# Kernel optimization log

Hardware: AMD Instinct MI355X
Metric: run time of the kernel (lower is better)

The kernel has to match this reference:

```python
import jax, jax.numpy as jnp
import numpy as np
import math

H = 16        # num query heads
KV = 4        # num key/value heads
HD = 128      # head_dim
THETA = 10000.0

def _rope(x, cos, sin):
    # x: [B, h, S, HD]; cos/sin: [1, 1, S, HD//2]
    xr, xi = x[..., :HD // 2], x[..., HD // 2:]
    return jnp.concatenate([xr * cos - xi * sin, xr * sin + xi * cos], axis=-1)

def setup_inputs() -> dict:
    key = jax.random.key(0)
    ks = jax.random.split(key, 5)
    B, S, D = 1, 4096, 2048
    s = 1.0 / math.sqrt(D)
    return {
        "hidden_states": jax.random.normal(ks[0], (B, S, D), jnp.float32),
        "Wq": jax.random.normal(ks[1], (D, H * HD), jnp.float32) * s,
        "Wk": jax.random.normal(ks[2], (D, KV * HD), jnp.float32) * s,
        "Wv": jax.random.normal(ks[3], (D, KV * HD), jnp.float32) * s,
        "Wo": jax.random.normal(ks[4], (H * HD, D), jnp.float32) * s,
    }

def reference(hidden_states, Wq, Wk, Wv, Wo):
    B, S, D = hidden_states.shape
    # projections -> [B, h, S, HD]
    q = (hidden_states @ Wq).reshape(B, S, H, HD).transpose(0, 2, 1, 3)
    k = (hidden_states @ Wk).reshape(B, S, KV, HD).transpose(0, 2, 1, 3)
    v = (hidden_states @ Wv).reshape(B, S, KV, HD).transpose(0, 2, 1, 3)
    # rotary embedding (half-split layout, matching the torch module)
    inv_freq = 1.0 / (THETA ** (jnp.arange(0, HD, 2, dtype=jnp.float32) / HD))
    freqs = jnp.arange(S, dtype=jnp.float32)[:, None] * inv_freq[None, :]  # [S, HD//2]
    cos = jnp.cos(freqs)[None, None]
    sin = jnp.sin(freqs)[None, None]
    q = _rope(q, cos, sin)
    k = _rope(k, cos, sin)
    # GQA: repeat KV heads to match query heads
    rep = H // KV
    k = jnp.repeat(k, rep, axis=1)
    v = jnp.repeat(v, rep, axis=1)
    # non-causal scaled dot-product attention (world_size==1 path)
    scores = jnp.einsum('bhqd,bhkd->bhqk', q, k) / math.sqrt(HD)
    w = jax.nn.softmax(scores, axis=-1)
    o = jnp.einsum('bhqk,bhkd->bhqd', w, v)
    o = o.transpose(0, 2, 1, 3).reshape(B, S, H * HD)
    return o @ Wo
```

## Files before the change

kernel.cpp:

```cpp
#include <hip/hip_runtime.h>
#include <math.h>

#define S_LEN 4096
#define D_MODEL 2048
#define N_HEADS 16
#define N_KV 4
#define HEAD_DIM 128
#define KV_D 512
#define QKV_N 3072
#define SM_SHIFT 18.0f

typedef short bf16x8 __attribute__((ext_vector_type(8)));
typedef float f32x4 __attribute__((ext_vector_type(4)));

#if __has_builtin(__builtin_amdgcn_exp2f)
#define EXP2(x) __builtin_amdgcn_exp2f(x)
#else
#define EXP2(x) exp2f(x)
#endif

static __device__ __forceinline__ unsigned short f2b(float f) {
  unsigned int u = __float_as_uint(f);
  unsigned int r = (u + 0x7FFFu + ((u >> 16) & 1u)) >> 16;
  return (unsigned short)r;
}
static __device__ __forceinline__ float b2f(unsigned short h) {
  return __uint_as_float(((unsigned int)h) << 16);
}
static __device__ __forceinline__ unsigned int cvt_pk_bf16(float a, float b) {
  unsigned int r;
  asm("v_cvt_pk_bf16_f32 %0, %1, %2" : "=v"(r) : "v"(a), "v"(b));
  return r;
}

static __device__ __forceinline__ void gload_lds16(const unsigned short* g,
                                                   unsigned short* l) {
  __builtin_amdgcn_global_load_lds(
      (const __attribute__((address_space(1))) void*)g,
      (__attribute__((address_space(3))) void*)l, 16, 0, 0);
}

__global__ __launch_bounds__(256) void prep_kernel(
    const float* __restrict__ X, const float* __restrict__ Wq,
    const float* __restrict__ Wk, const float* __restrict__ Wv,
    const float* __restrict__ Wo, unsigned short* __restrict__ Xb,
    unsigned short* __restrict__ Wqkv, unsigned short* __restrict__ WoT) {
  __shared__ float tile[32][33];
  const int b = blockIdx.x, t = threadIdx.x;
  if (b < 4096) {
    int i = b * 2048 + t * 8;
    float4 a = *(const float4*)(X + i);
    float4 v = *(const float4*)(X + i + 4);
    unsigned short tmp[8] = {f2b(a.x), f2b(a.y), f2b(a.z), f2b(a.w),
                             f2b(v.x), f2b(v.y), f2b(v.z), f2b(v.w)};
    *(uint4*)&Xb[i] = *(uint4*)tmp;
    return;
  }
  int id = b - 4096;
  const float* src;
  unsigned short* dst;
  int N, tc, rowOff;
  if (id < 4096) { src = Wq; dst = Wqkv; N = 2048; tc = 64; rowOff = 0; }
  else if (id < 5120) { id -= 4096; src = Wk; dst = Wqkv; N = 512; tc = 16; rowOff = 2048; }
  else if (id < 6144) { id -= 5120; src = Wv; dst = Wqkv; N = 512; tc = 16; rowOff = 2560; }
  else { id -= 6144; src = Wo; dst = WoT; N = 2048; tc = 64; rowOff = 0; }
  const int c0 = (id % tc) * 32, r0 = (id / tc) * 32;
  const int col = t & 31, rb = t >> 5;
#pragma unroll
  for (int i = 0; i < 4; i++)
    tile[rb + i * 8][col] = src[(size_t)(r0 + rb + i * 8) * N + c0 + col];
  __syncthreads();
#pragma unroll
  for (int i = 0; i < 4; i++)
    dst[(size_t)(rowOff + c0 + rb + i * 8) * 2048 + r0 + col] =
        f2b(tile[col][rb + i * 8]);
}

__global__ __launch_bounds__(256) void bgemm_kernel(
    const unsigned short* __restrict__ A, const unsigned short* __restrict__ Bt,
    void* __restrict__ C, int M, int N, int K, int bf16_out) {
  __shared__ unsigned short As[128 * 32];
  __shared__ unsigned short Bs[128 * 32];

  const int t = threadIdx.x;
  const int w = t >> 6, l = t & 63;
  const int quad = l >> 4, lx = l & 15;
  const int row0 = blockIdx.y * 128, col0 = blockIdx.x * 128;
  const int wr = (w >> 1) * 64, wc = (w & 1) * 64;

  f32x4 acc[4][4];
#pragma unroll
  for (int mt = 0; mt < 4; mt++)
#pragma unroll
    for (int nt = 0; nt < 4; nt++) acc[mt][nt] = (f32x4){0.f, 0.f, 0.f, 0.f};

  for (int kt = 0; kt < K; kt += 32) {
    __syncthreads();
#pragma unroll
    for (int j = 0; j < 2; j++) {
      int ch = w * 128 + j * 64 + l;
      int r = ch >> 2, kc = (ch & 3) * 8;
      gload_lds16(A + (size_t)(row0 + r) * K + kt + kc, &As[ch * 8]);
      gload_lds16(Bt + (size_t)(col0 + r) * K + kt + kc, &Bs[ch * 8]);
    }
    __syncthreads();

    bf16x8 af[4], bfr[4];
#pragma unroll
    for (int mt = 0; mt < 4; mt++)
      af[mt] = *(const bf16x8*)&As[(wr + mt * 16 + lx) * 32 + quad * 8];
#pragma unroll
    for (int nt = 0; nt < 4; nt++)
      bfr[nt] = *(const bf16x8*)&Bs[(wc + nt * 16 + lx) * 32 + quad * 8];
#pragma unroll
    for (int mt = 0; mt < 4; mt++)
#pragma unroll
      for (int nt = 0; nt < 4; nt++)
        acc[mt][nt] = __builtin_amdgcn_mfma_f32_16x16x32_bf16(af[mt], bfr[nt],
                                                              acc[mt][nt], 0, 0, 0);
  }

  if (bf16_out) {
    unsigned short* Cp = (unsigned short*)C;
#pragma unroll
    for (int mt = 0; mt < 4; mt++)
#pragma unroll
      for (int nt = 0; nt < 4; nt++)
#pragma unroll
        for (int r = 0; r < 4; r++) {
          int row = row0 + wr + mt * 16 + quad * 4 + r;
          int col = col0 + wc + nt * 16 + lx;
          Cp[(size_t)row * N + col] = f2b(acc[mt][nt][r]);
        }
  } else {
    float* Cp = (float*)C;
#pragma unroll
    for (int mt = 0; mt < 4; mt++)
#pragma unroll
      for (int nt = 0; nt < 4; nt++)
#pragma unroll
        for (int r = 0; r < 4; r++) {
          int row = row0 + wr + mt * 16 + quad * 4 + r;
          int col = col0 + wc + nt * 16 + lx;
          Cp[(size_t)row * N + col] = acc[mt][nt][r];
        }
  }
}

__global__ __launch_bounds__(256) void rope_kernel(unsigned short* __restrict__ QKV) {
  int id = blockIdx.x * 256 + threadIdx.x;
  int d = id & 63;
  int rem = id >> 6;
  int head = rem % 20;
  int s = rem / 20;
  unsigned short* p;
  float scale;
  if (head < N_HEADS) {
    p = QKV + (size_t)s * QKV_N + head * HEAD_DIM;
    scale = 0.12753139187f;
  } else {
    p = QKV + (size_t)s * QKV_N + 2048 + (head - N_HEADS) * HEAD_DIM;
    scale = 1.0f;
  }
  float inv = exp2f(-(float)d * (13.287712379549449f / 64.0f));
  float ang = (float)s * inv;
  float sn, c;
  sincosf(ang, &sn, &c);
  float xr = b2f(p[d]), xi = b2f(p[d + 64]);
  p[d] = f2b((xr * c - xi * sn) * scale);
  p[d + 64] = f2b((xr * sn + xi * c) * scale);
}

__global__ __launch_bounds__(256) void vtrans_kernel(
    const unsigned short* __restrict__ Vb, unsigned short* __restrict__ Vt) {
  __shared__ unsigned short tile[32][33];
  const int t = threadIdx.x;
  const int c0 = blockIdx.x * 32;
  const int s0 = blockIdx.y * 32;
  const int col = t & 31, rbase = t >> 5;
#pragma unroll
  for (int i = 0; i < 4; i++) {
    int row = rbase + i * 8;
    tile[row][col] = Vb[(size_t)(s0 + row) * QKV_N + c0 + col];
  }
  __syncthreads();
#pragma unroll
  for (int i = 0; i < 4; i++) {
    int row = rbase + i * 8;
    Vt[(size_t)(c0 + row) * S_LEN + s0 + col] = tile[col][row];
  }
}

__global__ __launch_bounds__(256, 2) void attn_kernel(
    const unsigned short* __restrict__ Qb, const unsigned short* __restrict__ Kb,
    const unsigned short* __restrict__ Vt, unsigned short* __restrict__ Ob) {
  __shared__ unsigned short Ks[2][64 * 128];
  __shared__ unsigned short Vs[2][128 * 64];
  __shared__ unsigned short Pt[4][32 * 64];

  const int t = threadIdx.x;
  const int wave = t >> 6;
  const int lane = t & 63;
  const int quad = lane >> 4;
  const int lx = lane & 15;
  const int lx7 = lx & 7;
  const int qt = blockIdx.x;
  const int h = blockIdx.y;
  const int kvh = h >> 2;

  const unsigned short* Kg = Kb + kvh * HEAD_DIM;
  const unsigned short* Vg = Vt + (size_t)(kvh * HEAD_DIM) * S_LEN;

  const unsigned short* Qg =
      Qb + (size_t)(qt * 128 + wave * 32) * QKV_N + h * HEAD_DIM;
  bf16x8 qf[2][4];
#pragma unroll
  for (int qs = 0; qs < 2; qs++)
#pragma unroll
    for (int ks = 0; ks < 4; ks++)
      qf[qs][ks] = *(const bf16x8*)(Qg + (size_t)(qs * 16 + lx) * QKV_N +
                                    (quad << 3) + (ks << 5));

  f32x4 oacc[2][8];
#pragma unroll
  for (int qs = 0; qs < 2; qs++)
#pragma unroll
    for (int dt = 0; dt < 8; dt++) oacc[qs][dt] = (f32x4){0.f, 0.f, 0.f, 0.f};
  float l_st[2] = {0.f, 0.f};

  const unsigned short* kgp[4];
  const unsigned short* vgp[4];
#pragma unroll
  for (int j = 0; j < 4; j++) {
    int ch = (j * 4 + wave) * 64 + lane;
    int r = ch >> 4, c = ch & 15;
    kgp[j] = Kg + (size_t)r * QKV_N + ((c ^ (r & 7)) << 3);
    int d = ch >> 3, c2 = ch & 7;
    vgp[j] = Vg + (size_t)d * S_LEN + ((c2 ^ (d & 7)) << 3);
  }

  auto stage = [&](int kt, int b) {
#pragma unroll
    for (int j = 0; j < 4; j++) {
      int ch = (j * 4 + wave) * 64 + lane;
      gload_lds16(kgp[j] + (size_t)kt * (64 * QKV_N), &Ks[b][ch * 8]);
    }
#pragma unroll
    for (int j = 0; j < 4; j++) {
      int ch = (j * 4 + wave) * 64 + lane;
      gload_lds16(vgp[j] + kt * 64, &Vs[b][ch * 8]);
    }
  };

  stage(0, 0);

  for (int kt = 0; kt < S_LEN / 64; kt++) {
    __syncthreads();
    if (kt + 1 < S_LEN / 64) stage(kt + 1, (kt + 1) & 1);
    const unsigned short* KsC = Ks[kt & 1];
    const unsigned short* VsC = Vs[kt & 1];

#pragma unroll
    for (int ksub = 0; ksub < 4; ksub++) {
      bf16x8 kf[4];
#pragma unroll
      for (int ks = 0; ks < 4; ks++)
        kf[ks] = *(const bf16x8*)&KsC[(ksub * 16 + lx) * 128 +
                                      (((ks * 4 + quad) ^ lx7) << 3)];
#pragma unroll
      for (int qs = 0; qs < 2; qs++) {
        f32x4 a = (f32x4){-SM_SHIFT, -SM_SHIFT, -SM_SHIFT, -SM_SHIFT};
        __builtin_amdgcn_s_setprio(1);
#pragma unroll
        for (int ks = 0; ks < 4; ks++)
          a = __builtin_amdgcn_mfma_f32_16x16x32_bf16(kf[ks], qf[qs][ks], a, 0, 0, 0);
        __builtin_amdgcn_s_setprio(0);
        float p0 = EXP2(a[0]);
        float p1 = EXP2(a[1]);
        float p2 = EXP2(a[2]);
        float p3 = EXP2(a[3]);
        l_st[qs] += (p0 + p1) + (p2 + p3);
        *(uint2*)&Pt[wave][(qs * 16 + lx) * 64 +
                           (((2 * ksub + (quad >> 1)) ^ lx7) << 3) +
                           ((quad & 1) << 2)] =
            make_uint2(cvt_pk_bf16(p0, p1), cvt_pk_bf16(p2, p3));
      }
    }

#pragma unroll
    for (int st = 0; st < 2; st++) {
      const int pc = ((st * 4 + quad) ^ lx7) << 3;
      bf16x8 pb0 = *(const bf16x8*)&Pt[wave][lx * 64 + pc];
      bf16x8 pb1 = *(const bf16x8*)&Pt[wave][(16 + lx) * 64 + pc];
      __builtin_amdgcn_s_setprio(1);
#pragma unroll
      for (int dt = 0; dt < 8; dt++) {
        bf16x8 vf = *(const bf16x8*)&VsC[(dt * 16 + lx) * 64 + pc];
        oacc[0][dt] = __builtin_amdgcn_mfma_f32_16x16x32_bf16(vf, pb0, oacc[0][dt], 0, 0, 0);
        oacc[1][dt] = __builtin_amdgcn_mfma_f32_16x16x32_bf16(vf, pb1, oacc[1][dt], 0, 0, 0);
      }
      __builtin_amdgcn_s_setprio(0);
    }
  }

#pragma unroll
  for (int qs = 0; qs < 2; qs++) {
    float l = l_st[qs];
    l += __shfl_xor(l, 16);
    l += __shfl_xor(l, 32);
    float linv = 1.0f / l;
    unsigned short* ob = Ob +
        (size_t)(qt * 128 + wave * 32 + qs * 16 + lx) * D_MODEL + h * HEAD_DIM +
        quad * 4;
#pragma unroll
    for (int dt = 0; dt < 8; dt++) {
      *(uint2*)&ob[dt * 16] = make_uint2(
          cvt_pk_bf16(oacc[qs][dt][0] * linv, oacc[qs][dt][1] * linv),
          cvt_pk_bf16(oacc[qs][dt][2] * linv, oacc[qs][dt][3] * linv));
    }
  }
}

extern "C" void kernel_launch(void* const* d_in, const int* in_sizes, int n_in,
                              void* d_out, int out_size, void* d_ws,
                              size_t ws_size, hipStream_t stream) {
  const float* X = (const float*)d_in[0];
  const float* Wq = (const float*)d_in[1];
  const float* Wk = (const float*)d_in[2];
  const float* Wv = (const float*)d_in[3];
  const float* Wo = (const float*)d_in[4];
  float* out = (float*)d_out;

  const size_t MB = 1048576;
  char* ws = (char*)d_ws;
  unsigned short* Xb    = (unsigned short*)ws;
  unsigned short* WqkvT = (unsigned short*)(ws + 16 * MB);
  unsigned short* WoT   = (unsigned short*)(ws + 28 * MB);
  unsigned short* QKV   = (unsigned short*)(ws + 36 * MB);
  unsigned short* Vtr   = (unsigned short*)(ws + 60 * MB);
  unsigned short* Ob    = (unsigned short*)(ws + 64 * MB);

  dim3 blk(256);
  prep_kernel<<<14336, blk, 0, stream>>>(X, Wq, Wk, Wv, Wo, Xb, WqkvT, WoT);
  bgemm_kernel<<<dim3(QKV_N / 128, S_LEN / 128), blk, 0, stream>>>(
      Xb, WqkvT, QKV, S_LEN, QKV_N, D_MODEL, 1);
  rope_kernel<<<(S_LEN * 20 * 64) / 256, blk, 0, stream>>>(QKV);
  vtrans_kernel<<<dim3(KV_D / 32, S_LEN / 32), blk, 0, stream>>>(QKV + 2560, Vtr);
  attn_kernel<<<dim3(S_LEN / 128, N_HEADS), blk, 0, stream>>>(
      QKV, QKV + 2048, Vtr, Ob);
  bgemm_kernel<<<dim3(D_MODEL / 128, S_LEN / 128), blk, 0, stream>>>(
      Ob, WoT, out, S_LEN, D_MODEL, D_MODEL, 0);
}
```

Measured before the change: 405.0 us.

## Split K/V waits in attention loop, fuse rope and V transpose, use hw bf16 convert

The attention main loop replaces __syncthreads with explicit vmcnt waits and raw barriers. Only the K half of the prefetched tile is waited on before QK^T, and V is waited on later, before the PV stage, so the V load overlaps the score computation. The rope and V-transpose kernels are merged into one launch, and the software float-to-bf16 rounding is replaced by the v_cvt_pk_bf16 instruction. The manual vmcnt counts depend on exact load ordering, so any compiler reordering or extra memory ops could break correctness.

Result: no change. 401.0 us (-1.0%).

```diff
diff --git a/kernel.cpp b/kernel.cpp
--- a/kernel.cpp
+++ b/kernel.cpp
@@ -19,11 +19,9 @@
 #define EXP2(x) exp2f(x)
 #endif
 
-static __device__ __forceinline__ unsigned short f2b(float f) {
-  unsigned int u = __float_as_uint(f);
-  unsigned int r = (u + 0x7FFFu + ((u >> 16) & 1u)) >> 16;
-  return (unsigned short)r;
-}
+#define SBAR() asm volatile("s_barrier" ::: "memory")
+#define VMCNT(n) asm volatile("s_waitcnt vmcnt(" #n ")" ::: "memory")
+
 static __device__ __forceinline__ float b2f(unsigned short h) {
   return __uint_as_float(((unsigned int)h) << 16);
 }
@@ -31,6 +29,9 @@
   unsigned int r;
   asm("v_cvt_pk_bf16_f32 %0, %1, %2" : "=v"(r) : "v"(a), "v"(b));
   return r;
+}
+static __device__ __forceinline__ unsigned short f2b(float f) {
+  return (unsigned short)cvt_pk_bf16(f, f);
 }
 
 static __device__ __forceinline__ void gload_lds16(const unsigned short* g,
@@ -51,8 +52,8 @@
     int i = b * 2048 + t * 8;
     float4 a = *(const float4*)(X + i);
     float4 v = *(const float4*)(X + i + 4);
-    unsigned short tmp[8] = {f2b(a.x), f2b(a.y), f2b(a.z), f2b(a.w),
-                             f2b(v.x), f2b(v.y), f2b(v.z), f2b(v.w)};
+    unsigned int tmp[4] = {cvt_pk_bf16(a.x, a.y), cvt_pk_bf16(a.z, a.w),
+                           cvt_pk_bf16(v.x, v.y), cvt_pk_bf16(v.z, v.w)};
     *(uint4*)&Xb[i] = *(uint4*)tmp;
     return;
   }
@@ -147,36 +148,38 @@
   }
 }
 
-__global__ __launch_bounds__(256) void rope_kernel(unsigned short* __restrict__ QKV) {
-  int id = blockIdx.x * 256 + threadIdx.x;
-  int d = id & 63;
-  int rem = id >> 6;
-  int head = rem % 20;
-  int s = rem / 20;
-  unsigned short* p;
-  float scale;
-  if (head < N_HEADS) {
-    p = QKV + (size_t)s * QKV_N + head * HEAD_DIM;
-    scale = 0.12753139187f;
-  } else {
-    p = QKV + (size_t)s * QKV_N + 2048 + (head - N_HEADS) * HEAD_DIM;
-    scale = 1.0f;
-  }
-  float inv = exp2f(-(float)d * (13.287712379549449f / 64.0f));
-  float ang = (float)s * inv;
-  float sn, c;
-  sincosf(ang, &sn, &c);
-  float xr = b2f(p[d]), xi = b2f(p[d + 64]);
-  p[d] = f2b((xr * c - xi * sn) * scale);
-  p[d + 64] = f2b((xr * sn + xi * c) * scale);
-}
-
-__global__ __launch_bounds__(256) void vtrans_kernel(
-    const unsigned short* __restrict__ Vb, unsigned short* __restrict__ Vt) {
+__global__ __launch_bounds__(256) void ropev_kernel(
+    unsigned short* __restrict__ QKV, unsigned short* __restrict__ Vt) {
+  const int t = threadIdx.x;
+  if (blockIdx.x < 20480) {
+    int id = blockIdx.x * 256 + t;
+    int d = id & 63;
+    int rem = id >> 6;
+    int head = rem % 20;
+    int s = rem / 20;
+    unsigned short* p;
+    float scale;
+    if (head < N_HEADS) {
+      p = QKV + (size_t)s * QKV_N + head * HEAD_DIM;
+      scale = 0.12753139187f;
+    } else {
+      p = QKV + (size_t)s * QKV_N + 2048 + (head - N_HEADS) * HEAD_DIM;
+      scale = 1.0f;
+    }
+    float inv = exp2f(-(float)d * (13.287712379549449f / 64.0f));
+    float ang = (float)s * inv;
+    float sn, c;
+    sincosf(ang, &sn, &c);
+    float xr = b2f(p[d]), xi = b2f(p[d + 64]);
+    p[d] = f2b((xr * c - xi * sn) * scale);
+    p[d + 64] = f2b((xr * sn + xi * c) * scale);
+    return;
+  }
   __shared__ unsigned short tile[32][33];
-  const int t = threadIdx.x;
-  const int c0 = blockIdx.x * 32;
-  const int s0 = blockIdx.y * 32;
+  const unsigned short* Vb = QKV + 2560;
+  int id = blockIdx.x - 20480;
+  const int c0 = (id & 15) * 32;
+  const int s0 = (id >> 4) * 32;
   const int col = t & 31, rbase = t >> 5;
 #pragma unroll
   for (int i = 0; i < 4; i++) {
@@ -255,7 +258,8 @@
   stage(0, 0);
 
   for (int kt = 0; kt < S_LEN / 64; kt++) {
-    __syncthreads();
+    VMCNT(4);
+    SBAR();
     if (kt + 1 < S_LEN / 64) stage(kt + 1, (kt + 1) & 1);
     const unsigned short* KsC = Ks[kt & 1];
     const unsigned short* VsC = Vs[kt & 1];
@@ -287,6 +291,9 @@
       }
     }
 
+    if (kt + 1 < S_LEN / 64) { VMCNT(8); } else { VMCNT(0); }
+    SBAR();
+
 #pragma unroll
     for (int st = 0; st < 2; st++) {
       const int pc = ((st * 4 + quad) ^ lx7) << 3;
@@ -344,8 +351,7 @@
   prep_kernel<<<14336, blk, 0, stream>>>(X, Wq, Wk, Wv, Wo, Xb, WqkvT, WoT);
   bgemm_kernel<<<dim3(QKV_N / 128, S_LEN / 128), blk, 0, stream>>>(
       Xb, WqkvT, QKV, S_LEN, QKV_N, D_MODEL, 1);
-  rope_kernel<<<(S_LEN * 20 * 64) / 256, blk, 0, stream>>>(QKV);
-  vtrans_kernel<<<dim3(KV_D / 32, S_LEN / 32), blk, 0, stream>>>(QKV + 2560, Vtr);
+  ropev_kernel<<<20480 + 2048, blk, 0, stream>>>(QKV, Vtr);
   attn_kernel<<<dim3(S_LEN / 128, N_HEADS), blk, 0, stream>>>(
       QKV, QKV + 2048, Vtr, Ob);
   bgemm_kernel<<<dim3(D_MODEL / 128, S_LEN / 128), blk, 0, stream>>>(
```
